# Optimization experiments

Hardware: AMD Instinct MI355X
Metric: run time of the kernel (lower is better)

## Reference

```python
import jax, jax.numpy as jnp
import numpy as np

B, F, C, H, W = 4, 16, 768, 16, 16   # video: b f c h w
L, M = 64, 16                        # audio: b c l m
NH = 12                              # num_heads
WS_V = 4                             # local_window (video window size, frames)
GROUPS = 32                          # GroupNorm32
EPS = 1e-5


def group_norm(x, scale, bias):
    # x: [b, c, t]; normalize over (channels-within-group, t)
    b, c, t = x.shape
    xg = x.reshape(b, GROUPS, c // GROUPS, t)
    mu = xg.mean(axis=(2, 3), keepdims=True)
    var = xg.var(axis=(2, 3), keepdims=True)
    xg = (xg - mu) * jax.lax.rsqrt(var + EPS)
    return xg.reshape(b, c, t) * scale[None, :, None] + bias[None, :, None]


def setup_inputs() -> dict:
    key = jax.random.key(0)
    ks = jax.random.split(key, 8)
    s = 0.02
    return {
        "video": jax.random.normal(ks[0], (B, F, C, H, W), jnp.float32),
        "audio": jax.random.normal(ks[1], (B, C, L, M), jnp.float32),
        "vn_scale": jnp.ones((C,), jnp.float32),
        "vn_bias": jnp.zeros((C,), jnp.float32),
        "an_scale": jnp.ones((C,), jnp.float32),
        "an_bias": jnp.zeros((C,), jnp.float32),
        "vqkv_w": jax.random.normal(ks[2], (3 * C, C), jnp.float32) * s,
        "vqkv_b": jnp.zeros((3 * C,), jnp.float32),
        "aqkv_w": jax.random.normal(ks[3], (3 * C, C), jnp.float32) * s,
        "aqkv_b": jnp.zeros((3 * C,), jnp.float32),
        "vproj_w": jax.random.normal(ks[4], (C, C), jnp.float32) * s,  # zero_module in orig; random for nontrivial baseline
        "vproj_b": jnp.zeros((C,), jnp.float32),
        "aproj_w": jax.random.normal(ks[5], (C, C), jnp.float32) * s,
        "aproj_b": jnp.zeros((C,), jnp.float32),
    }


def reference(video, audio, vn_scale, vn_bias, an_scale, an_bias,
              vqkv_w, vqkv_b, aqkv_w, aqkv_b,
              vproj_w, vproj_b, aproj_w, aproj_b):
    b, f, c, h, w = video.shape
    _, _, l, m = audio.shape
    ch = c // NH
    scale = ch ** -0.25
    ws_audio = WS_V * l // f
    nwin = f // WS_V
    wsv_tok = WS_V * h * w      # video tokens per window
    wsa_tok = ws_audio * m      # audio tokens per window

    vt = jnp.transpose(video, (0, 2, 1, 3, 4)).reshape(b, c, f * h * w)  # b c (f h w)
    at = audio.reshape(b, c, l * m)                                       # b c (l m)

    # 1x1 conv qkv after GroupNorm
    vqkv = jnp.einsum('oc,bct->bot', vqkv_w, group_norm(vt, vn_scale, vn_bias)) + vqkv_b[None, :, None]
    aqkv = jnp.einsum('oc,bct->bot', aqkv_w, group_norm(at, an_scale, an_bias)) + aqkv_b[None, :, None]
    q_v, k_v, v_v = jnp.split(vqkv, 3, axis=1)
    q_a, k_a, v_a = jnp.split(aqkv, 3, axis=1)

    # attention_index with window_shift = 0
    va_index = (jnp.arange(wsa_tok)[None, :] + (jnp.arange(nwin) * wsa_tok)[:, None]) % (l * m)
    av_index = (jnp.arange(wsv_tok)[None, :] + (jnp.arange(nwin) * wsv_tok)[:, None]) % (f * h * w)

    def heads(x):
        return x.reshape(b, NH, ch, -1)

    # video queries attend gathered audio windows
    qv = heads(q_v).reshape(b, NH, ch, nwin, wsv_tok)
    ka = jnp.take(heads(k_a), va_index, axis=-1)   # [b,NH,ch,nwin,wsa_tok]
    vav = jnp.take(heads(v_a), va_index, axis=-1)
    wts = jax.nn.softmax(jnp.einsum('bhcnt,bhcns->bhnts', qv * scale, ka * scale), axis=-1)
    v_out = jnp.einsum('bhnts,bhcns->bhcnt', wts, vav).reshape(b, c, f * h * w)

    # audio queries attend gathered video windows
    qa = heads(q_a).reshape(b, NH, ch, nwin, wsa_tok)
    kv = jnp.take(heads(k_v), av_index, axis=-1)   # [b,NH,ch,nwin,wsv_tok]
    vvv = jnp.take(heads(v_v), av_index, axis=-1)
    wts = jax.nn.softmax(jnp.einsum('bhcnt,bhcns->bhnts', qa * scale, kv * scale), axis=-1)
    a_out = jnp.einsum('bhnts,bhcns->bhcnt', wts, vvv).reshape(b, c, l * m)

    # zero-init 1x1x1 / 1x1 proj_out convs + residual
    vh = jnp.transpose(v_out.reshape(b, c, f, h, w), (0, 2, 1, 3, 4))  # b f c h w
    vh = jnp.einsum('oc,bfchw->bfohw', vproj_w, vh) + vproj_b[None, None, :, None, None]
    ah = jnp.einsum('oc,bclm->bolm', aproj_w, a_out.reshape(b, c, l, m)) + aproj_b[None, :, None, None]
    return video + vh, audio + ah
```

## Files before the change

kernel.cpp:

```cpp
#include <hip/hip_runtime.h>
#include <hip/hip_bf16.h>

typedef unsigned short ushort_t;
typedef __attribute__((ext_vector_type(8))) short short8;
typedef __attribute__((ext_vector_type(4))) float f32x4;
struct __align__(8) us4 { ushort_t x, y, z, w; };

#define DI __device__ __forceinline__

DI float b2f(unsigned int u16) {
  union { unsigned int i; float f; } v;
  v.i = u16 << 16;
  return v.f;
}
DI ushort_t f2b(float f) {
  union { float f; unsigned int u; } v; v.f = f;
  unsigned int r = v.u + 0x7FFFu + ((v.u >> 16) & 1u);
  return (ushort_t)(r >> 16);
}

DI void gl_lds16(const ushort_t* g, ushort_t* l) {
  __builtin_amdgcn_global_load_lds(
      (const __attribute__((address_space(1))) unsigned int*)g,
      (__attribute__((address_space(3))) unsigned int*)l, 16, 0, 0);
}

__global__ __launch_bounds__(256) void fused_pre_kernel(
    const float* __restrict__ video, const float* __restrict__ audio,
    float* __restrict__ part,
    const float* __restrict__ w0, const float* __restrict__ w1,
    const float* __restrict__ w2, const float* __restrict__ w3,
    ushort_t* __restrict__ o0, ushort_t* __restrict__ o1,
    ushort_t* __restrict__ o2, ushort_t* __restrict__ o3) {
  const int bid = blockIdx.x;
  const int tid = threadIdx.x;
  __shared__ float red[8];
  if (bid < 2560) {
    float s = 0.f, ss = 0.f;
    if (bid < 2048) {
      int bg = bid >> 4, f = bid & 15;
      int b = bg >> 5, g = bg & 31;
      const float4* base = reinterpret_cast<const float4*>(
          video + ((size_t)((b * 16 + f) * 768 + g * 24)) * 256);
#pragma unroll
      for (int i = 0; i < 6; ++i) {
        float4 v = base[i * 256 + tid];
        s += v.x + v.y + v.z + v.w;
        ss += v.x * v.x + v.y * v.y + v.z * v.z + v.w * v.w;
      }
    } else {
      int a = bid - 2048;
      int bg = a >> 2, p = a & 3;
      int b = bg >> 5, g = bg & 31;
      const float* ab = audio + ((size_t)(b * 768 + g * 24)) * 1024 + p * 256;
#pragma unroll
      for (int i = 0; i < 6; ++i) {
        int row = i * 4 + (tid >> 6);
        float4 v = *reinterpret_cast<const float4*>(ab + (size_t)row * 1024 + (tid & 63) * 4);
        s += v.x + v.y + v.z + v.w;
        ss += v.x * v.x + v.y * v.y + v.z * v.z + v.w * v.w;
      }
    }
    for (int off = 32; off > 0; off >>= 1) { s += __shfl_down(s, off, 64); ss += __shfl_down(ss, off, 64); }
    int wv = tid >> 6, ln = tid & 63;
    if (ln == 0) { red[wv * 2] = s; red[wv * 2 + 1] = ss; }
    __syncthreads();
    if (tid == 0) {
      part[bid * 2] = red[0] + red[2] + red[4] + red[6];
      part[bid * 2 + 1] = red[1] + red[3] + red[5] + red[7];
    }
  } else {
    const int n1 = (2304 * 768) / 4, n3 = (768 * 768) / 4;
    const int total = 2 * n1 + 2 * n3;
    int wb = bid - 2560;
    for (int i = wb * 256 + tid; i < total; i += 1024 * 256) {
      const float4* src;
      ushort_t* dst;
      int j;
      if (i < n1) { src = (const float4*)w0; dst = o0; j = i; }
      else if (i < 2 * n1) { src = (const float4*)w1; dst = o1; j = i - n1; }
      else if (i < 2 * n1 + n3) { src = (const float4*)w2; dst = o2; j = i - 2 * n1; }
      else { src = (const float4*)w3; dst = o3; j = i - 2 * n1 - n3; }
      float4 v = src[j];
      us4 o = {f2b(v.x), f2b(v.y), f2b(v.z), f2b(v.w)};
      *reinterpret_cast<us4*>(dst + (size_t)j * 4) = o;
    }
  }
}

__global__ __launch_bounds__(256) void norm_fused_kernel(
    const float* __restrict__ video, const float* __restrict__ audio,
    const float* __restrict__ part,
    const float* __restrict__ vsc, const float* __restrict__ vbi,
    const float* __restrict__ asc, const float* __restrict__ abi,
    ushort_t* __restrict__ Xv, ushort_t* __restrict__ Xa) {
  __shared__ float T[32][257];
  __shared__ float shA[32], shB[32];
  const int bx = blockIdx.x;
  const int tid = threadIdx.x;
  if (bx < 1536) {
    const int bf = bx / 24, ct = bx % 24;
    const int b = bf >> 4, f = bf & 15;
    const int c0 = ct * 32;
    if (tid < 32) {
      int c = c0 + tid, g = c / 24;
      float s = 0.f, ss = 0.f;
#pragma unroll
      for (int i = 0; i < 16; ++i) {
        s += part[((b * 32 + g) * 16 + i) * 2];
        ss += part[((b * 32 + g) * 16 + i) * 2 + 1];
      }
      const float N = 24.f * 4096.f;
      float m = s / N;
      float r = rsqrtf(ss / N - m * m + 1e-5f);
      float A = r * vsc[c];
      shA[tid] = A;
      shB[tid] = vbi[c] - m * A;
    }
    __syncthreads();
#pragma unroll
    for (int i = 0; i < 8; ++i) {
      int idx = i * 256 + tid;
      int c = idx >> 6, q4 = idx & 63;
      float4 v = *reinterpret_cast<const float4*>(
          video + ((size_t)((b * 16 + f) * 768 + c0 + c)) * 256 + q4 * 4);
      float A = shA[c], B = shB[c];
      float4 o = {A * v.x + B, A * v.y + B, A * v.z + B, A * v.w + B};
      *reinterpret_cast<float4*>(&T[c][q4 * 4]) = o;
    }
    __syncthreads();
#pragma unroll
    for (int i = 0; i < 8; ++i) {
      int idx = i * 256 + tid;
      int c4 = idx & 7, hw = idx >> 3;
      us4 o = {f2b(T[c4 * 4 + 0][hw]), f2b(T[c4 * 4 + 1][hw]),
               f2b(T[c4 * 4 + 2][hw]), f2b(T[c4 * 4 + 3][hw])};
      *reinterpret_cast<us4*>(Xv + ((size_t)(b * 4096 + f * 256 + hw)) * 768 + c0 + c4 * 4) = o;
    }
  } else {
    const int ax = bx - 1536;
    const int bt = ax / 24, ct = ax % 24;
    const int b = bt >> 2, t0 = (bt & 3) * 256;
    const int c0 = ct * 32;
    if (tid < 32) {
      int c = c0 + tid, g = c / 24;
      float s = 0.f, ss = 0.f;
#pragma unroll
      for (int i = 0; i < 4; ++i) {
        s += part[(2048 + (b * 32 + g) * 4 + i) * 2];
        ss += part[(2048 + (b * 32 + g) * 4 + i) * 2 + 1];
      }
      const float N = 24.f * 1024.f;
      float m = s / N;
      float r = rsqrtf(ss / N - m * m + 1e-5f);
      float A = r * asc[c];
      shA[tid] = A;
      shB[tid] = abi[c] - m * A;
    }
    __syncthreads();
#pragma unroll
    for (int i = 0; i < 8; ++i) {
      int idx = i * 256 + tid;
      int c = idx >> 6, q4 = idx & 63;
      float4 v = *reinterpret_cast<const float4*>(
          audio + ((size_t)(b * 768 + c0 + c)) * 1024 + t0 + q4 * 4);
      float A = shA[c], B = shB[c];
      float4 o = {A * v.x + B, A * v.y + B, A * v.z + B, A * v.w + B};
      *reinterpret_cast<float4*>(&T[c][q4 * 4]) = o;
    }
    __syncthreads();
#pragma unroll
    for (int i = 0; i < 8; ++i) {
      int idx = i * 256 + tid;
      int c4 = idx & 7, tt = idx >> 3;
      us4 o = {f2b(T[c4 * 4 + 0][tt]), f2b(T[c4 * 4 + 1][tt]),
               f2b(T[c4 * 4 + 2][tt]), f2b(T[c4 * 4 + 3][tt])};
      *reinterpret_cast<us4*>(Xa + ((size_t)(b * 1024 + t0 + tt)) * 768 + c0 + c4 * 4) = o;
    }
  }
}

__global__ __launch_bounds__(256) void qkv_fused_kernel(
    const ushort_t* __restrict__ Xv, const ushort_t* __restrict__ Xa,
    const ushort_t* __restrict__ Wqv, const ushort_t* __restrict__ Wqa,
    const float* __restrict__ vqkv_b, const float* __restrict__ aqkv_b,
    ushort_t* __restrict__ Qv, ushort_t* __restrict__ Kv, ushort_t* __restrict__ Vv,
    ushort_t* __restrict__ Qa, ushort_t* __restrict__ Ka, ushort_t* __restrict__ Va) {
  __shared__ ushort_t sm[32768];
  const int bid = blockIdx.x;
  const int tid = threadIdx.x;
  const int lane = tid & 63, wave = tid >> 6;
  const int quad = lane >> 4, l16 = lane & 15;

  const bool isv = bid < 2304;
  const int lb = isv ? bid : bid - 2304;
  const int nwg = isv ? 2304 : 576;
  const ushort_t* A = isv ? Xv : Xa;
  const ushort_t* W = isv ? Wqv : Wqa;
  const float* bias = isv ? vqkv_b : aqkv_b;
  ushort_t* pQ = isv ? Qv : Qa;
  ushort_t* pK = isv ? Kv : Ka;
  ushort_t* pV = isv ? Vv : Va;
  const int M = isv ? 16384 : 4096;

  const int lid = (lb & 7) * (nwg >> 3) + (lb >> 3);
  const int n0 = (lid % 18) * 128, m0 = (lid / 18) * 128;
  const int wm = (wave & 1) * 64, wn = (wave >> 1) * 64;

  const int srow = wave * 32 + (lane >> 3);
  const int sq = ((lane & 7) ^ (lane >> 3)) * 8;
  const ushort_t* gA = A + (size_t)(m0 + srow) * 768 + sq;
  const ushort_t* gB = W + (size_t)(n0 + srow) * 768 + sq;

  f32x4 acc[4][4];
#pragma unroll
  for (int i = 0; i < 4; ++i)
#pragma unroll
    for (int j = 0; j < 4; ++j) acc[i][j] = (f32x4){0.f, 0.f, 0.f, 0.f};

  auto stage = [&](int kc, int cur) {
    ushort_t* lA = sm + cur * 8192 + wave * 2048;
    ushort_t* lB = sm + 16384 + cur * 8192 + wave * 2048;
#pragma unroll
    for (int i = 0; i < 4; ++i) {
      gl_lds16(gA + (size_t)i * 8 * 768 + kc, lA + i * 512);
      gl_lds16(gB + (size_t)i * 8 * 768 + kc, lB + i * 512);
    }
  };

  stage(0, 0);
  __syncthreads();
  int cur = 0;
  for (int t = 0; t < 12; ++t) {
    if (t < 11) stage((t + 1) * 64, cur ^ 1);
    const ushort_t* cA = sm + cur * 8192;
    const ushort_t* cB = sm + 16384 + cur * 8192;
#pragma unroll
    for (int ks = 0; ks < 2; ++ks) {
      short8 av[4], bv[4];
#pragma unroll
      for (int im = 0; im < 4; ++im) {
        int rr = wm + im * 16 + l16;
        av[im] = *reinterpret_cast<const short8*>(
            cA + rr * 64 + (((ks * 4 + quad) ^ (rr & 7)) * 8));
      }
#pragma unroll
      for (int in = 0; in < 4; ++in) {
        int rr = wn + in * 16 + l16;
        bv[in] = *reinterpret_cast<const short8*>(
            cB + rr * 64 + (((ks * 4 + quad) ^ (rr & 7)) * 8));
      }
#pragma unroll
      for (int im = 0; im < 4; ++im)
#pragma unroll
        for (int in = 0; in < 4; ++in)
          acc[im][in] = __builtin_amdgcn_mfma_f32_16x16x32_bf16(av[im], bv[in], acc[im][in], 0, 0, 0);
    }
    __syncthreads();
    cur ^= 1;
  }

  ushort_t* sC = sm;
  const int section = n0 / 768;
  const int obase = n0 - section * 768;
  if (section < 2) {
    const float qs = (section == 0) ? 0.125f * 1.44269504088896340736f : 1.0f;
#pragma unroll
    for (int in = 0; in < 4; ++in) {
      int ol = wn + in * 16 + l16;
      float bv_ = bias[n0 + ol];
#pragma unroll
      for (int im = 0; im < 4; ++im)
#pragma unroll
        for (int r = 0; r < 4; ++r) {
          int row = wm + im * 16 + quad * 4 + r;
          sC[row * 136 + ol] = f2b((acc[im][in][r] + bv_) * qs);
        }
    }
    __syncthreads();
    ushort_t* dst = (section == 0) ? pQ : pK;
#pragma unroll
    for (int i = 0; i < 8; ++i) {
      int cid = i * 256 + tid;
      int row = cid >> 4, ch = cid & 15;
      *reinterpret_cast<uint4*>(dst + (size_t)(m0 + row) * 768 + obase + ch * 8) =
          *reinterpret_cast<const uint4*>(sC + row * 136 + ch * 8);
    }
  } else {
#pragma unroll
    for (int in = 0; in < 4; ++in) {
      int ol = wn + in * 16 + l16;
      float bv_ = bias[n0 + ol];
#pragma unroll
      for (int im = 0; im < 4; ++im)
#pragma unroll
        for (int r = 0; r < 4; ++r) {
          int mr = wm + im * 16 + quad * 4 + r;
          sC[ol * 136 + mr] = f2b(acc[im][in][r] + bv_);
        }
    }
    __syncthreads();
#pragma unroll
    for (int i = 0; i < 8; ++i) {
      int cid = i * 256 + tid;
      int o = cid >> 4, ch = cid & 15;
      *reinterpret_cast<uint4*>(pV + (size_t)(obase + o) * M + m0 + ch * 8) =
          *reinterpret_cast<const uint4*>(sC + o * 136 + ch * 8);
    }
  }
}

__global__ __launch_bounds__(256) void proj_fused_kernel(
    const ushort_t* __restrict__ Ov, const ushort_t* __restrict__ Oa,
    const ushort_t* __restrict__ Wpv, const ushort_t* __restrict__ Wpa,
    const float* __restrict__ vproj_b, const float* __restrict__ aproj_b,
    float* __restrict__ out_v, const float* __restrict__ video,
    float* __restrict__ out_a, const float* __restrict__ audio) {
  __shared__ ushort_t sm[32768];
  const int bid = blockIdx.x;
  const int tid = threadIdx.x;
  const int lane = tid & 63, wave = tid >> 6;
  const int quad = lane >> 4, l16 = lane & 15;

  const bool isv = bid < 768;
  const int lb = isv ? bid : bid - 768;
  const int nwg = isv ? 768 : 192;
  const ushort_t* A = isv ? Ov : Oa;
  const ushort_t* W = isv ? Wpv : Wpa;
  const float* bias = isv ? vproj_b : aproj_b;
  float* outp = isv ? out_v : out_a;
  const float* resp = isv ? video : audio;

  const int lid = (lb & 7) * (nwg >> 3) + (lb >> 3);
  const int n0 = (lid % 6) * 128, m0 = (lid / 6) * 128;
  const int wm = (wave & 1) * 64, wn = (wave >> 1) * 64;

  const int srow = wave * 32 + (lane >> 3);
  const int sq = ((lane & 7) ^ (lane >> 3)) * 8;
  const ushort_t* gA = A + (size_t)(m0 + srow) * 768 + sq;
  const ushort_t* gB = W + (size_t)(n0 + srow) * 768 + sq;

  f32x4 acc[4][4];
#pragma unroll
  for (int i = 0; i < 4; ++i)
#pragma unroll
    for (int j = 0; j < 4; ++j) acc[i][j] = (f32x4){0.f, 0.f, 0.f, 0.f};

  auto stage = [&](int kc, int cur) {
    ushort_t* lA = sm + cur * 8192 + wave * 2048;
    ushort_t* lB = sm + 16384 + cur * 8192 + wave * 2048;
#pragma unroll
    for (int i = 0; i < 4; ++i) {
      gl_lds16(gA + (size_t)i * 8 * 768 + kc, lA + i * 512);
      gl_lds16(gB + (size_t)i * 8 * 768 + kc, lB + i * 512);
    }
  };

  stage(0, 0);
  __syncthreads();
  int cur = 0;
  for (int t = 0; t < 12; ++t) {
    if (t < 11) stage((t + 1) * 64, cur ^ 1);
    const ushort_t* cA = sm + cur * 8192;
    const ushort_t* cB = sm + 16384 + cur * 8192;
#pragma unroll
    for (int ks = 0; ks < 2; ++ks) {
      short8 av[4], bv[4];
#pragma unroll
      for (int im = 0; im < 4; ++im) {
        int rr = wm + im * 16 + l16;
        av[im] = *reinterpret_cast<const short8*>(
            cA + rr * 64 + (((ks * 4 + quad) ^ (rr & 7)) * 8));
      }
#pragma unroll
      for (int in = 0; in < 4; ++in) {
        int rr = wn + in * 16 + l16;
        bv[in] = *reinterpret_cast<const short8*>(
            cB + rr * 64 + (((ks * 4 + quad) ^ (rr & 7)) * 8));
      }
#pragma unroll
      for (int im = 0; im < 4; ++im)
#pragma unroll
        for (int in = 0; in < 4; ++in)
          acc[im][in] = __builtin_amdgcn_mfma_f32_16x16x32_bf16(av[im], bv[in], acc[im][in], 0, 0, 0);
    }
    __syncthreads();
    cur ^= 1;
  }

  ushort_t* sC = sm;
#pragma unroll
  for (int in = 0; in < 4; ++in) {
    int ol = wn + in * 16 + l16;
    float bv_ = bias[n0 + ol];
#pragma unroll
    for (int im = 0; im < 4; ++im)
#pragma unroll
      for (int r = 0; r < 4; ++r) {
        int mr = wm + im * 16 + quad * 4 + r;
        sC[ol * 136 + mr] = f2b(acc[im][in][r] + bv_);
      }
  }
  __syncthreads();
#pragma unroll
  for (int i = 0; i < 16; ++i) {
    int cid = i * 256 + tid;
    int o = cid >> 5, ch = cid & 31;
    uint2 pk = *reinterpret_cast<const uint2*>(sC + o * 136 + ch * 4);
    size_t gidx;
    if (isv) {
      int b = m0 >> 12, f = (m0 >> 8) & 15, hw0 = m0 & 255;
      gidx = ((size_t)((b * 16 + f) * 768 + n0 + o)) * 256 + hw0 + ch * 4;
    } else {
      int b = m0 >> 10, t0 = m0 & 1023;
      gidx = ((size_t)(b * 768 + n0 + o)) * 1024 + t0 + ch * 4;
    }
    float4 rv = *reinterpret_cast<const float4*>(resp + gidx);
    float4 ov;
    ov.x = rv.x + b2f(pk.x & 0xffff);
    ov.y = rv.y + b2f(pk.x >> 16);
    ov.z = rv.z + b2f(pk.y & 0xffff);
    ov.w = rv.w + b2f(pk.y >> 16);
    *reinterpret_cast<float4*>(outp + gidx) = ov;
  }
}

__global__ __launch_bounds__(256) void attn_fused_kernel(
    const ushort_t* __restrict__ Qv, const ushort_t* __restrict__ Ka,
    const ushort_t* __restrict__ Va, ushort_t* __restrict__ Ov,
    const ushort_t* __restrict__ Qa, const ushort_t* __restrict__ Kv,
    const ushort_t* __restrict__ Vv, ushort_t* __restrict__ Oa) {
  __shared__ ushort_t sm[25088];
  ushort_t* sK = sm;
  ushort_t* sV = sm + 8192;
  ushort_t* sP = sm + 16384;
  ushort_t* sQ = sP;
  const int tid = threadIdx.x;
  const int lane = tid & 63, wave = tid >> 6;
  const int quad = lane >> 4, l16 = lane & 15;

  const int bx0 = blockIdx.x;
  const bool isv = bx0 >= 768;
  int lb;
  if (isv) {
    int local = bx0 - 768;
    lb = (local & 7) * 384 + (local >> 3);
  } else {
    int local = bx0;
    lb = (local & 7) * 96 + (local >> 3);
  }

  const ushort_t* Qt = isv ? Qv : Qa;
  const ushort_t* Kt = isv ? Ka : Kv;
  const ushort_t* Vc = isv ? Va : Vv;
  ushort_t* Ot = isv ? Ov : Oa;
  const int qlog = isv ? 4 : 2;
  const int NT = isv ? 2 : 8;
  const int QW = isv ? 1024 : 256;
  const int SW = isv ? 256 : 1024;
  const int TQb = isv ? 4096 : 1024;
  const int TSb = isv ? 1024 : 4096;
  const int Ms = isv ? 4096 : 16384;

  const int qt = lb & ((1 << qlog) - 1);
  const int win = (lb >> qlog) & 3;
  const int whb = lb >> (qlog + 2);
  const int h = whb % 12;
  const int batch = whb / 12;
  const int hc = h * 64;
  const int nq0 = batch * TQb + win * QW + qt * 64;
  const int ns_base = batch * TSb + win * SW;

  const int r8 = lane >> 3, c8 = lane & 7;
  const int s8 = (c8 ^ r8) * 8;
  const int r16 = lane >> 4, c16 = lane & 15;

  auto stage_k = [&](int ns0) {
#pragma unroll
    for (int i = 0; i < 4; ++i) {
      int row = wave * 32 + i * 8 + r8;
      gl_lds16(Kt + (size_t)(ns0 + row) * 768 + hc + s8, sK + (wave * 32 + i * 8) * 64);
    }
  };
  auto stage_v = [&](int ns0) {
#pragma unroll
    for (int i = 0; i < 4; ++i) {
      int ch = wave * 16 + i * 4 + r16;
      int slot = c16 ^ (i * 4 + r16);
      gl_lds16(Vc + (size_t)(hc + ch) * Ms + ns0 + slot * 8, sV + (wave * 16 + i * 4) * 128);
    }
  };

#pragma unroll
  for (int i = 0; i < 2; ++i) {
    int row = wave * 16 + i * 8 + r8;
    gl_lds16(Qt + (size_t)(nq0 + row) * 768 + hc + s8, sQ + (wave * 16 + i * 8) * 64);
  }
  stage_k(ns_base);
  stage_v(ns_base);
  __syncthreads();

  short8 qf[2];
#pragma unroll
  for (int ks = 0; ks < 2; ++ks)
    qf[ks] = *reinterpret_cast<const short8*>(
        sQ + (wave * 16 + l16) * 64 + (((ks * 4 + quad) ^ (l16 & 7)) * 8));

  const short8 vones = {0x3F80, 0x3F80, 0x3F80, 0x3F80, 0x3F80, 0x3F80, 0x3F80, 0x3F80};

  float mr[4];
  f32x4 on[4], onl;
#pragma unroll
  for (int r = 0; r < 4; ++r) mr[r] = -1e30f;
#pragma unroll
  for (int nc = 0; nc < 4; ++nc) on[nc] = (f32x4){0.f, 0.f, 0.f, 0.f};
  onl = (f32x4){0.f, 0.f, 0.f, 0.f};
  const int prow0 = (wave * 16 + quad * 4) * 136;

  for (int t = 0; t < NT; ++t) {
    f32x4 sf[8];
#pragma unroll
    for (int nt = 0; nt < 8; ++nt) sf[nt] = (f32x4){0.f, 0.f, 0.f, 0.f};
#pragma unroll
    for (int ks = 0; ks < 2; ++ks) {
#pragma unroll
      for (int nt = 0; nt < 8; ++nt) {
        short8 kf = *reinterpret_cast<const short8*>(
            sK + (nt * 16 + l16) * 64 + (((ks * 4 + quad) ^ (l16 & 7)) * 8));
        sf[nt] = __builtin_amdgcn_mfma_f32_16x16x32_bf16(qf[ks], kf, sf[nt], 0, 0, 0);
      }
    }
    __syncthreads();
    if (t + 1 < NT) stage_k(ns_base + (t + 1) * 128);
#pragma unroll
    for (int r = 0; r < 4; ++r) {
      float m_ = fmaxf(fmaxf(sf[0][r], sf[1][r]), sf[2][r]);
      m_ = fmaxf(fmaxf(m_, sf[3][r]), sf[4][r]);
      m_ = fmaxf(fmaxf(m_, sf[5][r]), sf[6][r]);
      m_ = fmaxf(m_, sf[7][r]);
#pragma unroll
      for (int off = 1; off < 16; off <<= 1) m_ = fmaxf(m_, __shfl_xor(m_, off));
      float mnew = fmaxf(mr[r], m_);
      float al = __builtin_amdgcn_exp2f(mr[r] - mnew);
      mr[r] = mnew;
      int prow = prow0 + r * 136;
#pragma unroll
      for (int nt = 0; nt < 8; ++nt) {
        float p = __builtin_amdgcn_exp2f(sf[nt][r] - mnew);
        sP[prow + nt * 16 + l16] = (ushort_t)((__float_as_uint(p) + 0x8000u) >> 16);
      }
#pragma unroll
      for (int nc = 0; nc < 4; ++nc) on[nc][r] *= al;
      onl[r] *= al;
    }
#pragma unroll
    for (int ks = 0; ks < 4; ++ks) {
      short8 pf = *reinterpret_cast<const short8*>(sP + (wave * 16 + l16) * 136 + ks * 32 + quad * 8);
#pragma unroll
      for (int nc = 0; nc < 4; ++nc) {
        short8 vf = *reinterpret_cast<const short8*>(
            sV + (nc * 16 + l16) * 128 + (((ks * 4 + quad) ^ l16) * 8));
        on[nc] = __builtin_amdgcn_mfma_f32_16x16x32_bf16(pf, vf, on[nc], 0, 0, 0);
      }
      onl = __builtin_amdgcn_mfma_f32_16x16x32_bf16(pf, vones, onl, 0, 0, 0);
    }
    if (t + 1 < NT) {
      __syncthreads();
      stage_v(ns_base + (t + 1) * 128);
    }
  }
#pragma unroll
  for (int r = 0; r < 4; ++r) {
    float inv = 1.f / onl[r];
    int prow = prow0 + r * 136;
#pragma unroll
    for (int nc = 0; nc < 4; ++nc)
      sP[prow + nc * 16 + l16] = f2b(on[nc][r] * inv);
  }
  __syncthreads();
#pragma unroll
  for (int i = 0; i < 2; ++i) {
    int c = i * 256 + tid;
    int row = c >> 3, cc = c & 7;
    *reinterpret_cast<uint4*>(Ot + (size_t)(nq0 + row) * 768 + hc + cc * 8) =
        *reinterpret_cast<const uint4*>(sP + row * 136 + cc * 8);
  }
}

extern "C" void kernel_launch(void* const* d_in, const int* in_sizes, int n_in,
                              void* d_out, int out_size, void* d_ws, size_t ws_size,
                              hipStream_t stream) {
  (void)in_sizes; (void)n_in; (void)out_size; (void)ws_size;
  const float* video = (const float*)d_in[0];
  const float* audio = (const float*)d_in[1];
  const float* vn_s = (const float*)d_in[2];
  const float* vn_b = (const float*)d_in[3];
  const float* an_s = (const float*)d_in[4];
  const float* an_b = (const float*)d_in[5];
  const float* vqkv_w = (const float*)d_in[6];
  const float* vqkv_b = (const float*)d_in[7];
  const float* aqkv_w = (const float*)d_in[8];
  const float* aqkv_b = (const float*)d_in[9];
  const float* vproj_w = (const float*)d_in[10];
  const float* vproj_b = (const float*)d_in[11];
  const float* aproj_w = (const float*)d_in[12];
  const float* aproj_b = (const float*)d_in[13];

  float* out_v = (float*)d_out;
  float* out_a = out_v + (size_t)4 * 16 * 768 * 16 * 16;

  char* ws = (char*)d_ws;
  size_t off = 0;
  auto carve = [&](size_t bytes) {
    char* p = ws + off;
    off += (bytes + 255) & ~(size_t)255;
    return p;
  };
  float* part = (float*)carve(2560 * 2 * 4);
  ushort_t* Xv = (ushort_t*)carve((size_t)16384 * 768 * 2);
  ushort_t* Xa = (ushort_t*)carve((size_t)4096 * 768 * 2);
  ushort_t* Wqv = (ushort_t*)carve((size_t)2304 * 768 * 2);
  ushort_t* Wqa = (ushort_t*)carve((size_t)2304 * 768 * 2);
  ushort_t* Wpv = (ushort_t*)carve((size_t)768 * 768 * 2);
  ushort_t* Wpa = (ushort_t*)carve((size_t)768 * 768 * 2);
  ushort_t* Qv = (ushort_t*)carve((size_t)16384 * 768 * 2);
  ushort_t* Kv = (ushort_t*)carve((size_t)16384 * 768 * 2);
  ushort_t* Vv = (ushort_t*)carve((size_t)16384 * 768 * 2);
  ushort_t* Qa = (ushort_t*)carve((size_t)4096 * 768 * 2);
  ushort_t* Ka = (ushort_t*)carve((size_t)4096 * 768 * 2);
  ushort_t* Va = (ushort_t*)carve((size_t)4096 * 768 * 2);
  ushort_t* Ov = Xv;
  ushort_t* Oa = Xa;

  fused_pre_kernel<<<3584, 256, 0, stream>>>(video, audio, part,
                                             vqkv_w, aqkv_w, vproj_w, aproj_w,
                                             Wqv, Wqa, Wpv, Wpa);
  norm_fused_kernel<<<1920, 256, 0, stream>>>(video, audio, part,
                                              vn_s, vn_b, an_s, an_b, Xv, Xa);
  qkv_fused_kernel<<<2880, 256, 0, stream>>>(Xv, Xa, Wqv, Wqa, vqkv_b, aqkv_b,
                                             Qv, Kv, Vv, Qa, Ka, Va);
  attn_fused_kernel<<<3840, 256, 0, stream>>>(Qv, Ka, Va, Ov, Qa, Kv, Vv, Oa);
  proj_fused_kernel<<<960, 256, 0, stream>>>(Ov, Oa, Wpv, Wpa, vproj_b, aproj_b,
                                             out_v, video, out_a, audio);
}
```

Baseline: 324.9 us.

## Double attention block to 128 query rows sharing K/V tiles, add MFMA priority

```diff
diff --git a/kernel.cpp b/kernel.cpp
--- a/kernel.cpp
+++ b/kernel.cpp
@@ -425,36 +425,38 @@
   }
 }
 
-__global__ __launch_bounds__(256) void attn_fused_kernel(
+__global__ __launch_bounds__(512) void attn_fused_kernel(
     const ushort_t* __restrict__ Qv, const ushort_t* __restrict__ Ka,
     const ushort_t* __restrict__ Va, ushort_t* __restrict__ Ov,
     const ushort_t* __restrict__ Qa, const ushort_t* __restrict__ Kv,
     const ushort_t* __restrict__ Vv, ushort_t* __restrict__ Oa) {
-  __shared__ ushort_t sm[25088];
+  __shared__ ushort_t sm[33792];
   ushort_t* sK = sm;
   ushort_t* sV = sm + 8192;
   ushort_t* sP = sm + 16384;
-  ushort_t* sQ = sP;
   const int tid = threadIdx.x;
   const int lane = tid & 63, wave = tid >> 6;
   const int quad = lane >> 4, l16 = lane & 15;
+  const int half = wave >> 2, w4 = wave & 3;
+  ushort_t* sPh = sP + half * 8704;
+  ushort_t* sQh = sPh;
 
   const int bx0 = blockIdx.x;
-  const bool isv = bx0 >= 768;
+  const bool isv = bx0 >= 384;
   int lb;
   if (isv) {
-    int local = bx0 - 768;
-    lb = (local & 7) * 384 + (local >> 3);
+    int local = bx0 - 384;
+    lb = (local & 7) * 192 + (local >> 3);
   } else {
     int local = bx0;
-    lb = (local & 7) * 96 + (local >> 3);
+    lb = (local & 7) * 48 + (local >> 3);
   }
 
   const ushort_t* Qt = isv ? Qv : Qa;
   const ushort_t* Kt = isv ? Ka : Kv;
   const ushort_t* Vc = isv ? Va : Vv;
   ushort_t* Ot = isv ? Ov : Oa;
-  const int qlog = isv ? 4 : 2;
+  const int qlog = isv ? 3 : 1;
   const int NT = isv ? 2 : 8;
   const int QW = isv ? 1024 : 256;
   const int SW = isv ? 256 : 1024;
@@ -468,7 +470,7 @@
   const int h = whb % 12;
   const int batch = whb / 12;
   const int hc = h * 64;
-  const int nq0 = batch * TQb + win * QW + qt * 64;
+  const int nq0 = batch * TQb + win * QW + qt * 128;
   const int ns_base = batch * TSb + win * SW;
 
   const int r8 = lane >> 3, c8 = lane & 7;
@@ -477,24 +479,26 @@
 
   auto stage_k = [&](int ns0) {
 #pragma unroll
-    for (int i = 0; i < 4; ++i) {
-      int row = wave * 32 + i * 8 + r8;
-      gl_lds16(Kt + (size_t)(ns0 + row) * 768 + hc + s8, sK + (wave * 32 + i * 8) * 64);
+    for (int i = 0; i < 2; ++i) {
+      int rbase = wave * 16 + i * 8;
+      gl_lds16(Kt + (size_t)(ns0 + rbase + r8) * 768 + hc + s8, sK + rbase * 64);
     }
   };
   auto stage_v = [&](int ns0) {
 #pragma unroll
-    for (int i = 0; i < 4; ++i) {
-      int ch = wave * 16 + i * 4 + r16;
-      int slot = c16 ^ (i * 4 + r16);
-      gl_lds16(Vc + (size_t)(hc + ch) * Ms + ns0 + slot * 8, sV + (wave * 16 + i * 4) * 128);
+    for (int i = 0; i < 2; ++i) {
+      int cbase = wave * 8 + i * 4;
+      int ch = cbase + r16;
+      int slot = c16 ^ (ch & 15);
+      gl_lds16(Vc + (size_t)(hc + ch) * Ms + ns0 + slot * 8, sV + cbase * 128);
     }
   };
 
 #pragma unroll
   for (int i = 0; i < 2; ++i) {
-    int row = wave * 16 + i * 8 + r8;
-    gl_lds16(Qt + (size_t)(nq0 + row) * 768 + hc + s8, sQ + (wave * 16 + i * 8) * 64);
+    int rbase = wave * 16 + i * 8;
+    gl_lds16(Qt + (size_t)(nq0 + rbase + r8) * 768 + hc + s8,
+             sP + (rbase >> 6) * 8704 + (rbase & 63) * 64);
   }
   stage_k(ns_base);
   stage_v(ns_base);
@@ -504,7 +508,7 @@
 #pragma unroll
   for (int ks = 0; ks < 2; ++ks)
     qf[ks] = *reinterpret_cast<const short8*>(
-        sQ + (wave * 16 + l16) * 64 + (((ks * 4 + quad) ^ (l16 & 7)) * 8));
+        sQh + (w4 * 16 + l16) * 64 + (((ks * 4 + quad) ^ (l16 & 7)) * 8));
 
   const short8 vones = {0x3F80, 0x3F80, 0x3F80, 0x3F80, 0x3F80, 0x3F80, 0x3F80, 0x3F80};
 
@@ -515,12 +519,13 @@
 #pragma unroll
   for (int nc = 0; nc < 4; ++nc) on[nc] = (f32x4){0.f, 0.f, 0.f, 0.f};
   onl = (f32x4){0.f, 0.f, 0.f, 0.f};
-  const int prow0 = (wave * 16 + quad * 4) * 136;
+  const int prow0 = (w4 * 16 + quad * 4) * 136;
 
   for (int t = 0; t < NT; ++t) {
     f32x4 sf[8];
 #pragma unroll
     for (int nt = 0; nt < 8; ++nt) sf[nt] = (f32x4){0.f, 0.f, 0.f, 0.f};
+    __builtin_amdgcn_s_setprio(1);
 #pragma unroll
     for (int ks = 0; ks < 2; ++ks) {
 #pragma unroll
@@ -530,6 +535,7 @@
         sf[nt] = __builtin_amdgcn_mfma_f32_16x16x32_bf16(qf[ks], kf, sf[nt], 0, 0, 0);
       }
     }
+    __builtin_amdgcn_s_setprio(0);
     __syncthreads();
     if (t + 1 < NT) stage_k(ns_base + (t + 1) * 128);
 #pragma unroll
@@ -547,15 +553,16 @@
 #pragma unroll
       for (int nt = 0; nt < 8; ++nt) {
         float p = __builtin_amdgcn_exp2f(sf[nt][r] - mnew);
-        sP[prow + nt * 16 + l16] = (ushort_t)((__float_as_uint(p) + 0x8000u) >> 16);
+        sPh[prow + nt * 16 + l16] = (ushort_t)((__float_as_uint(p) + 0x8000u) >> 16);
       }
 #pragma unroll
       for (int nc = 0; nc < 4; ++nc) on[nc][r] *= al;
       onl[r] *= al;
     }
+    __builtin_amdgcn_s_setprio(1);
 #pragma unroll
     for (int ks = 0; ks < 4; ++ks) {
-      short8 pf = *reinterpret_cast<const short8*>(sP + (wave * 16 + l16) * 136 + ks * 32 + quad * 8);
+      short8 pf = *reinterpret_cast<const short8*>(sPh + (w4 * 16 + l16) * 136 + ks * 32 + quad * 8);
 #pragma unroll
       for (int nc = 0; nc < 4; ++nc) {
         short8 vf = *reinterpret_cast<const short8*>(
@@ -564,6 +571,7 @@
       }
       onl = __builtin_amdgcn_mfma_f32_16x16x32_bf16(pf, vones, onl, 0, 0, 0);
     }
+    __builtin_amdgcn_s_setprio(0);
     if (t + 1 < NT) {
       __syncthreads();
       stage_v(ns_base + (t + 1) * 128);
@@ -575,15 +583,15 @@
     int prow = prow0 + r * 136;
 #pragma unroll
     for (int nc = 0; nc < 4; ++nc)
-      sP[prow + nc * 16 + l16] = f2b(on[nc][r] * inv);
+      sPh[prow + nc * 16 + l16] = f2b(on[nc][r] * inv);
   }
   __syncthreads();
 #pragma unroll
   for (int i = 0; i < 2; ++i) {
-    int c = i * 256 + tid;
+    int c = i * 512 + tid;
     int row = c >> 3, cc = c & 7;
     *reinterpret_cast<uint4*>(Ot + (size_t)(nq0 + row) * 768 + hc + cc * 8) =
-        *reinterpret_cast<const uint4*>(sP + row * 136 + cc * 8);
+        *reinterpret_cast<const uint4*>(sP + (row >> 6) * 8704 + (row & 63) * 136 + cc * 8);
   }
 }
 
@@ -639,7 +647,7 @@
                                               vn_s, vn_b, an_s, an_b, Xv, Xa);
   qkv_fused_kernel<<<2880, 256, 0, stream>>>(Xv, Xa, Wqv, Wqa, vqkv_b, aqkv_b,
                                              Qv, Kv, Vv, Qa, Ka, Va);
-  attn_fused_kernel<<<3840, 256, 0, stream>>>(Qv, Ka, Va, Ov, Qa, Kv, Vv, Oa);
+  attn_fused_kernel<<<1920, 512, 0, stream>>>(Qv, Ka, Va, Ov, Qa, Kv, Vv, Oa);
   proj_fused_kernel<<<960, 256, 0, stream>>>(Ov, Oa, Wpv, Wpa, vproj_b, aproj_b,
                                              out_v, video, out_a, audio);
 }
```

New measurement: 321.9 us. Within noise of the previous version (-0.9%).
